# Kernel tuning notes

Hardware: AMD Instinct MI355X
Metric: run time of the kernel (lower is better)

Reference implementation:

```python
import jax, jax.numpy as jnp
import numpy as np

# Dims
B_, L_, IN_ = 16, 8192, 57
DM, DS, HD, EXP, NL, OUT = 64, 32, 32, 2, 2, 6
DI = EXP * DM            # 128 inner dim
NH = DI // HD            # 4 heads
DPROJ = 2 * DI + 2 * DS + NH  # z, x, B, C, dt


def setup_inputs() -> dict:
    key = jax.random.key(0)
    ks = jax.random.split(key, 8)
    def rn(k, shape, scale=0.02):
        return jax.random.normal(k, shape, dtype=jnp.float32) * scale
    return {
        "x": jax.random.normal(ks[0], (B_, L_, IN_), dtype=jnp.float32),
        "W_in": rn(ks[1], (IN_, DM)),
        "b_in": jnp.zeros((DM,), jnp.float32),
        "in_proj_W": rn(ks[2], (NL, DM, DPROJ)),
        "in_proj_b": jnp.zeros((NL, DPROJ), jnp.float32),
        "A_log": jnp.log(jnp.broadcast_to(jnp.arange(1, NH + 1, dtype=jnp.float32), (NL, NH))),
        "D": jnp.ones((NL, NH), jnp.float32),
        "dt_bias": rn(ks[3], (NL, NH), 0.1),
        "out_proj_W": rn(ks[4], (NL, DI, DM)),
        "out_proj_b": jnp.zeros((NL, DM), jnp.float32),
        "cls_W": rn(ks[5], (DM, OUT)),
        "cls_b": jnp.zeros((OUT,), jnp.float32),
    }


def _mamba_layer(x, W, b, A_log, D, dt_bias, Wo, bo):
    """SISO Mamba3-style selective scan block. x: [B, L, DM]."""
    Bsz, L, _ = x.shape
    zxbcdt = x @ W + b                               # [B, L, DPROJ]
    z, xin, Bm, Cm, dt = jnp.split(
        zxbcdt, [DI, 2 * DI, 2 * DI + DS, 2 * DI + 2 * DS], axis=-1)
    dt = jax.nn.softplus(dt + dt_bias)               # [B, L, NH]
    A = -jnp.exp(A_log)                              # [NH], per-head scalar (SISO)
    xin = jax.nn.silu(xin).reshape(Bsz, L, NH, HD)   # [B, L, NH, HD]
    Bm = jax.nn.silu(Bm)                             # [B, L, DS]
    Cm = jax.nn.silu(Cm)                             # [B, L, DS]
    decay = jnp.exp(dt * A)                          # [B, L, NH]

    def step(h, inp):
        # h: [B, NH, HD, DS]
        xt, bt, ct, dtt, dect = inp
        h = dect[:, :, None, None] * h + (dtt[:, :, None] * xt)[..., None] * bt[:, None, None, :]
        yt = jnp.einsum('bhpn,bn->bhp', h, ct)       # [B, NH, HD]
        return h, yt

    h0 = jnp.zeros((Bsz, NH, HD, DS), x.dtype)
    xs = (jnp.moveaxis(xin, 1, 0), jnp.moveaxis(Bm, 1, 0), jnp.moveaxis(Cm, 1, 0),
          jnp.moveaxis(dt, 1, 0), jnp.moveaxis(decay, 1, 0))
    _, ys = jax.lax.scan(step, h0, xs)               # [L, B, NH, HD]
    y = jnp.moveaxis(ys, 0, 1) + D[None, None, :, None] * xin
    y = y.reshape(Bsz, L, DI) * jax.nn.silu(z)       # gated output
    return y @ Wo + bo                               # [B, L, DM]


def reference(x, W_in, b_in, in_proj_W, in_proj_b, A_log, D, dt_bias,
              out_proj_W, out_proj_b, cls_W, cls_b):
    h = x @ W_in + b_in                              # linear_in
    for l in range(NL):                              # residual Mamba stack
        h = h + _mamba_layer(h, in_proj_W[l], in_proj_b[l], A_log[l], D[l],
                             dt_bias[l], out_proj_W[l], out_proj_b[l])
    pooled = h.mean(axis=1)                          # AdaptiveAvgPool1d(1)
    return pooled @ cls_W + cls_b                    # classifier [B, OUT]
```

## Files before the change

### kernel.cpp

```cpp
#include <hip/hip_runtime.h>

#define BSZ   16
#define LSEQ  8192
#define DMDL  64
#define DSD   32
#define HDD   32
#define NHD   4
#define DIN   128
#define NLAY  2
#define NOUTC 6
#define DPRJ  324
#define QC    64
#define NCH   128
#define NT21  21

typedef __attribute__((ext_vector_type(8))) short bf16x8;
typedef __attribute__((ext_vector_type(4))) float f32x4;

__device__ float          g_h0[BSZ*LSEQ*DMDL];
__device__ unsigned short g_xy[BSZ*LSEQ*DIN];
__device__ unsigned short g_Ba[BSZ*LSEQ*DSD];
__device__ unsigned short g_Ca[BSZ*LSEQ*DSD];
__device__ float          g_dt[BSZ*LSEQ*NHD];
__device__ float          g_pc[BSZ*LSEQ*NHD];
__device__ float          g_cS[BSZ*NCH*NHD*HDD*DSD];
__device__ unsigned short g_Hb[BSZ*NCH*NHD*HDD*DSD];
__device__ float          g_cL[BSZ*NCH*NHD];
__device__ float          g_ppc[BSZ*NCH*DMDL];
__device__ unsigned short g_wf[NLAY*NT21*2*64*8];
__device__ unsigned short g_wo[NLAY*4*4*64*8];

__device__ __forceinline__ float silu_f(float v){ return v / (1.0f + __expf(-v)); }
__device__ __forceinline__ float softplus_f(float v){ return (v > 15.0f) ? v : __logf(1.0f + __expf(v)); }
__device__ __forceinline__ unsigned short f2bf(float f){
  union { float f; unsigned u; } v; v.f = f;
  unsigned r = v.u + 0x7FFFu + ((v.u >> 16) & 1u);
  return (unsigned short)(r >> 16);
}
__device__ __forceinline__ float bf2f(unsigned short h){
  union { unsigned u; float f; } v; v.u = ((unsigned)h) << 16;
  return v.f;
}

__global__ __launch_bounds__(256) void k_linin(
    const float* __restrict__ x, const float* __restrict__ W,
    const float* __restrict__ bias)
{
  __shared__ float xs[64*60];
  __shared__ float wl[57*64];
  const int tid = threadIdx.x;
  const long tb = (long)blockIdx.x * 64;
  for (int i = tid; i < 64*57; i += 256){
    int t = i / 57, k = i - t*57;
    xs[t*60 + k] = x[tb*57 + i];
  }
  for (int i = tid; i < 57*64; i += 256) wl[i] = W[i];
  __syncthreads();
  const int t0 = (tid >> 4) * 4, d0 = (tid & 15) * 4;
  float acc[4][4];
  #pragma unroll
  for (int i = 0; i < 4; ++i)
    #pragma unroll
    for (int j = 0; j < 4; ++j) acc[i][j] = 0.f;
  for (int k = 0; k < 57; ++k){
    float4 w4 = *(const float4*)&wl[k*64 + d0];
    float wv[4] = {w4.x, w4.y, w4.z, w4.w};
    #pragma unroll
    for (int i = 0; i < 4; ++i){
      float xv = xs[(t0+i)*60 + k];
      #pragma unroll
      for (int j = 0; j < 4; ++j) acc[i][j] += xv * wv[j];
    }
  }
  float4 b4 = *(const float4*)&bias[d0];
  float bv[4] = {b4.x, b4.y, b4.z, b4.w};
  #pragma unroll
  for (int i = 0; i < 4; ++i){
    float4 o;
    o.x = acc[i][0] + bv[0]; o.y = acc[i][1] + bv[1];
    o.z = acc[i][2] + bv[2]; o.w = acc[i][3] + bv[3];
    *(float4*)&g_h0[(tb + t0 + i)*64 + d0] = o;
  }
}

__global__ __launch_bounds__(128) void k_wprep(const float* __restrict__ W)
{
  const int nt = blockIdx.x;
  const int l  = blockIdx.y;
  const int ks = threadIdx.x >> 6, lane = threadIdx.x & 63;
  const float* Wl = W + (long)l*64*DPRJ;
  const int n  = nt*16 + (lane & 15);
  const int k0 = ks*32 + (lane >> 4)*8;
  unsigned short v[8];
  #pragma unroll
  for (int j = 0; j < 8; ++j)
    v[j] = (n < DPRJ) ? f2bf(Wl[(k0 + j)*DPRJ + n]) : (unsigned short)0;
  unsigned short* d = &g_wf[((((long)l*NT21 + nt)*2 + ks)*64 + lane)*8];
  *(ushort4*)&d[0] = make_ushort4(v[0], v[1], v[2], v[3]);
  *(ushort4*)&d[4] = make_ushort4(v[4], v[5], v[6], v[7]);
}

__global__ __launch_bounds__(64) void k_wprep2(const float* __restrict__ Wo)
{
  const int nt = blockIdx.x >> 2, ks = blockIdx.x & 3, l = blockIdx.y;
  const int lane = threadIdx.x;
  const int n  = nt*16 + (lane & 15);
  const int k0 = ks*32 + (lane >> 4)*8;
  const float* Wl = Wo + (long)l*128*64;
  unsigned short* d = &g_wo[((((long)l*4 + nt)*4 + ks)*64 + lane)*8];
  unsigned short v[8];
  #pragma unroll
  for (int j = 0; j < 8; ++j) v[j] = f2bf(Wl[(k0 + j)*64 + n]);
  *(ushort4*)&d[0] = make_ushort4(v[0], v[1], v[2], v[3]);
  *(ushort4*)&d[4] = make_ushort4(v[4], v[5], v[6], v[7]);
}

#define OP 136
__global__ __launch_bounds__(256) void k_proj(
    const float* __restrict__ bias, const float* __restrict__ dt_bias, int l)
{
  __shared__ __align__(16) unsigned short Afr[8*2*64*8];
  __shared__ __align__(16) unsigned short Obuf[128*OP];
  const int tid = threadIdx.x;
  const long tb = (long)blockIdx.x * 128;
  #pragma unroll
  for (int r = 0; r < 4; ++r){
    const int c = tid + 256*r;
    const int t = c >> 3, k8 = c & 7;
    float4 f0 = *(const float4*)&g_h0[(tb + t)*64 + k8*8];
    float4 f1 = *(const float4*)&g_h0[(tb + t)*64 + k8*8 + 4];
    const int mt = t >> 4, ks = k8 >> 2, q = k8 & 3, ln = (t & 15) + 16*q;
    unsigned short* d = &Afr[(((mt*2 + ks)*64) + ln)*8];
    *(ushort4*)&d[0] = make_ushort4(f2bf(f0.x), f2bf(f0.y), f2bf(f0.z), f2bf(f0.w));
    *(ushort4*)&d[4] = make_ushort4(f2bf(f1.x), f2bf(f1.y), f2bf(f1.z), f2bf(f1.w));
  }
  __syncthreads();
  const int w = tid >> 6, lane = tid & 63;
  const int colq = lane & 15, rowq = lane >> 4;
  bf16x8 a[2][2];
  #pragma unroll
  for (int m = 0; m < 2; ++m)
    #pragma unroll
    for (int ks = 0; ks < 2; ++ks)
      a[m][ks] = *(const bf16x8*)&Afr[((((2*w + m)*2 + ks)*64) + lane)*8];
  const float* bl = bias + (long)l*DPRJ;
  const unsigned short* wf = &g_wf[(long)l*NT21*2*64*8];
  #pragma unroll
  for (int nti = 0; nti < 8; ++nti){
    const int nt = 8 + nti;
    bf16x8 b0 = *(const bf16x8*)&wf[((nt*2 + 0)*64 + lane)*8];
    bf16x8 b1 = *(const bf16x8*)&wf[((nt*2 + 1)*64 + lane)*8];
    const float b = bl[nt*16 + colq];
    #pragma unroll
    for (int m = 0; m < 2; ++m){
      f32x4 acc = {0.f, 0.f, 0.f, 0.f};
      acc = __builtin_amdgcn_mfma_f32_16x16x32_bf16(a[m][0], b0, acc, 0, 0, 0);
      acc = __builtin_amdgcn_mfma_f32_16x16x32_bf16(a[m][1], b1, acc, 0, 0, 0);
      const int tbase = (2*w + m)*16 + rowq*4;
      const int ocol = nti*16 + colq;
      #pragma unroll
      for (int r = 0; r < 4; ++r)
        Obuf[(tbase + r)*OP + ocol] = f2bf(silu_f(acc[r] + b));
    }
  }
  __syncthreads();
  #pragma unroll
  for (int it = 0; it < 8; ++it){
    const int i = tid + 256*it;
    const int t = i >> 4, c0 = (i & 15) * 8;
    *(uint4*)&g_xy[(tb + t)*128 + c0] = *(const uint4*)&Obuf[t*OP + c0];
  }
  __syncthreads();
  #pragma unroll
  for (int nti = 0; nti < 4; ++nti){
    const int nt = 16 + nti;
    bf16x8 b0 = *(const bf16x8*)&wf[((nt*2 + 0)*64 + lane)*8];
    bf16x8 b1 = *(const bf16x8*)&wf[((nt*2 + 1)*64 + lane)*8];
    const float b = bl[nt*16 + colq];
    #pragma unroll
    for (int m = 0; m < 2; ++m){
      f32x4 acc = {0.f, 0.f, 0.f, 0.f};
      acc = __builtin_amdgcn_mfma_f32_16x16x32_bf16(a[m][0], b0, acc, 0, 0, 0);
      acc = __builtin_amdgcn_mfma_f32_16x16x32_bf16(a[m][1], b1, acc, 0, 0, 0);
      const int tbase = (2*w + m)*16 + rowq*4;
      const int ocol = nti*16 + colq;
      #pragma unroll
      for (int r = 0; r < 4; ++r)
        Obuf[(tbase + r)*OP + ocol] = f2bf(silu_f(acc[r] + b));
    }
  }
  {
    bf16x8 b0 = *(const bf16x8*)&wf[((20*2 + 0)*64 + lane)*8];
    bf16x8 b1 = *(const bf16x8*)&wf[((20*2 + 1)*64 + lane)*8];
    #pragma unroll
    for (int m = 0; m < 2; ++m){
      f32x4 acc = {0.f, 0.f, 0.f, 0.f};
      acc = __builtin_amdgcn_mfma_f32_16x16x32_bf16(a[m][0], b0, acc, 0, 0, 0);
      acc = __builtin_amdgcn_mfma_f32_16x16x32_bf16(a[m][1], b1, acc, 0, 0, 0);
      if (colq < 4){
        const int tbase = (2*w + m)*16 + rowq*4;
        const float b = bl[320 + colq] + dt_bias[l*4 + colq];
        #pragma unroll
        for (int r = 0; r < 4; ++r)
          g_dt[(tb + tbase + r)*4 + colq] = softplus_f(acc[r] + b);
      }
    }
  }
  __syncthreads();
  #pragma unroll
  for (int it = 0; it < 4; ++it){
    const int i = tid + 256*it;
    const int t = i >> 3, k = i & 7;
    const int c0 = (k & 3) * 8;
    if (k < 4){
      *(uint4*)&g_Ba[(tb + t)*32 + c0] = *(const uint4*)&Obuf[t*OP + c0];
    } else {
      *(uint4*)&g_Ca[(tb + t)*32 + c0] = *(const uint4*)&Obuf[t*OP + 32 + c0];
    }
  }
}

#define SB 40
#define ST 72
__global__ __launch_bounds__(256) void k_s1(
    const float* __restrict__ A_log, const float* __restrict__ Dp, int l)
{
  __shared__ __align__(16) unsigned short u_bc[2*64*SB];
  __shared__ __align__(16) unsigned short Bbt[32*ST];
  __shared__ __align__(16) unsigned short Mb[64*ST];
  __shared__ float Sl[4*64];
  __shared__ float dts[4*64];
  __shared__ float wls[4*64];
  const int tid = threadIdx.x;
  const int cI = blockIdx.x, b = blockIdx.y;
  const long tb = (long)b*LSEQ + (long)cI*QC;
  unsigned short* Bb = u_bc;
  unsigned short* Cb = u_bc + 64*SB;
  for (int i = tid; i < 512; i += 256){
    const int s = i >> 3, n0 = (i & 7) * 4;
    ushort4 bu = *(const ushort4*)&g_Ba[(tb + s)*32 + n0];
    ushort4 cu = *(const ushort4*)&g_Ca[(tb + s)*32 + n0];
    *(ushort4*)&Bb[s*SB + n0] = bu;
    *(ushort4*)&Cb[s*SB + n0] = cu;
    Bbt[(n0    )*ST + s] = bu.x;
    Bbt[(n0 + 1)*ST + s] = bu.y;
    Bbt[(n0 + 2)*ST + s] = bu.z;
    Bbt[(n0 + 3)*ST + s] = bu.w;
  }
  {
    const int h = tid >> 6, t = tid & 63;
    const float Ah = -__expf(A_log[l*4 + h]);
    const float v = g_dt[(tb + t)*4 + h];
    float x = v * Ah;
    #pragma unroll
    for (int d = 1; d < 64; d <<= 1){
      float y = __shfl_up(x, d);
      if (t >= d) x += y;
    }
    Sl[h*64 + t] = x;
    dts[h*64 + t] = v;
    const float send = __shfl(x, 63);
    wls[h*64 + t] = __expf(send - x) * v;
    if (t == 63) g_cL[((long)b*NCH + cI)*4 + h] = x;
    g_pc[(tb + t)*4 + h] = __expf(x);
  }
  __syncthreads();
  const int w = tid >> 6, lane = tid & 63;
  const int colq = lane & 15, rowq = lane >> 4;
  float Greg[3][4];
  int Gmt[3], Gst[3];
  #pragma unroll
  for (int rep = 0; rep < 3; ++rep){
    const int k = w + rep*4;
    if (k < 10){
      const int mt = (k >= 6) ? 3 : ((k >= 3) ? 2 : ((k >= 1) ? 1 : 0));
      const int st = k - mt*(mt+1)/2;
      Gmt[rep] = mt; Gst[rep] = st;
      bf16x8 af = *(const bf16x8*)&Cb[(mt*16 + colq)*SB + rowq*8];
      bf16x8 bf = *(const bf16x8*)&Bb[(st*16 + colq)*SB + rowq*8];
      f32x4 acc = {0.f, 0.f, 0.f, 0.f};
      acc = __builtin_amdgcn_mfma_f32_16x16x32_bf16(af, bf, acc, 0, 0, 0);
      #pragma unroll
      for (int r = 0; r < 4; ++r) Greg[rep][r] = acc[r];
    } else { Gmt[rep] = -1; Gst[rep] = 0; }
  }
  #pragma unroll
  for (int rep = 0; rep < 2; ++rep){
    const int k = w + rep*4;
    if (k < 6){
      const int mt = (k < 3) ? 0 : ((k < 5) ? 1 : 2);
      const int st = (k < 3) ? (k + 1) : ((k < 5) ? (k - 1) : 3);
      #pragma unroll
      for (int r = 0; r < 4; ++r)
        Mb[(mt*16 + rowq*4 + r)*ST + st*16 + colq] = 0;
    }
  }
  unsigned short* Xt  = u_bc;
  unsigned short* Xwt = u_bc + 32*ST;
  for (int h = 0; h < NHD; ++h){
    __syncthreads();
    for (int i = tid; i < 512; i += 256){
      const int s = i >> 3, p0 = (i & 7) * 4;
      ushort4 u = *(const ushort4*)&g_xy[(tb + s)*128 + h*32 + p0];
      const float wv = wls[h*64 + s];
      Xt[(p0    )*ST + s] = u.x;  Xwt[(p0    )*ST + s] = f2bf(wv * bf2f(u.x));
      Xt[(p0 + 1)*ST + s] = u.y;  Xwt[(p0 + 1)*ST + s] = f2bf(wv * bf2f(u.y));
      Xt[(p0 + 2)*ST + s] = u.z;  Xwt[(p0 + 2)*ST + s] = f2bf(wv * bf2f(u.z));
      Xt[(p0 + 3)*ST + s] = u.w;  Xwt[(p0 + 3)*ST + s] = f2bf(wv * bf2f(u.w));
    }
    #pragma unroll
    for (int rep = 0; rep < 3; ++rep){
      if (Gmt[rep] >= 0){
        const int mt = Gmt[rep], st = Gst[rep];
        const int s = st*16 + colq;
        const float sls = Sl[h*64 + s];
        const float dv = dts[h*64 + s];
        #pragma unroll
        for (int r = 0; r < 4; ++r){
          const int t = mt*16 + rowq*4 + r;
          const float m = (s <= t) ? __expf(Sl[h*64 + t] - sls) * dv * Greg[rep][r] : 0.f;
          Mb[t*ST + s] = f2bf(m);
        }
      }
    }
    __syncthreads();
    const float Dh = Dp[l*4 + h];
    {
      bf16x8 a0 = *(const bf16x8*)&Mb[(w*16 + colq)*ST + rowq*8];
      bf16x8 a1 = *(const bf16x8*)&Mb[(w*16 + colq)*ST + 32 + rowq*8];
      #pragma unroll
      for (int nt = 0; nt < 2; ++nt){
        bf16x8 b0 = *(const bf16x8*)&Xt[(nt*16 + colq)*ST + rowq*8];
        bf16x8 b1 = *(const bf16x8*)&Xt[(nt*16 + colq)*ST + 32 + rowq*8];
        f32x4 acc = {0.f, 0.f, 0.f, 0.f};
        acc = __builtin_amdgcn_mfma_f32_16x16x32_bf16(a0, b0, acc, 0, 0, 0);
        acc = __builtin_amdgcn_mfma_f32_16x16x32_bf16(a1, b1, acc, 0, 0, 0);
        const int p = nt*16 + colq;
        #pragma unroll
        for (int r = 0; r < 4; ++r){
          const int t = w*16 + rowq*4 + r;
          const float xv = bf2f(Xt[p*ST + t]);
          g_xy[(tb + t)*128 + h*32 + p] = f2bf(acc[r] + Dh*xv);
        }
      }
    }
    {
      const int mt = w & 1, nt = w >> 1;
      bf16x8 a0 = *(const bf16x8*)&Xwt[(mt*16 + colq)*ST + rowq*8];
      bf16x8 a1 = *(const bf16x8*)&Xwt[(mt*16 + colq)*ST + 32 + rowq*8];
      bf16x8 b0 = *(const bf16x8*)&Bbt[(nt*16 + colq)*ST + rowq*8];
      bf16x8 b1 = *(const bf16x8*)&Bbt[(nt*16 + colq)*ST + 32 + rowq*8];
      f32x4 acc = {0.f, 0.f, 0.f, 0.f};
      acc = __builtin_amdgcn_mfma_f32_16x16x32_bf16(a0, b0, acc, 0, 0, 0);
      acc = __builtin_amdgcn_mfma_f32_16x16x32_bf16(a1, b1, acc, 0, 0, 0);
      const long base = (((long)b*NCH + cI)*NHD + h)*(HDD*DSD);
      const int n = nt*16 + colq;
      #pragma unroll
      for (int r = 0; r < 4; ++r){
        const int p = mt*16 + rowq*4 + r;
        g_cS[base + p*32 + n] = acc[r];
      }
    }
  }
}

__global__ __launch_bounds__(128) void k_s2()
{
  const int h = blockIdx.x >> 3, seg = blockIdx.x & 7, b = blockIdx.y;
  const int idx = seg*128 + threadIdx.x;
  float H = 0.f;
  for (int c = 0; c < NCH; ++c){
    const long o = (((long)b*NCH + c)*NHD + h)*1024 + idx;
    const float cs = g_cS[o];
    const float lg = g_cL[((long)b*NCH + c)*4 + h];
    g_Hb[o] = f2bf(H);
    H = __expf(lg) * H + cs;
  }
}

__global__ __launch_bounds__(256) void k_s3(
    const float* __restrict__ ipb, const float* __restrict__ bo, int l, int finalLayer)
{
  __shared__ __align__(16) unsigned short Hb[128*40];
  __shared__ __align__(16) unsigned short Cb[64*40];
  __shared__ __align__(16) unsigned short gl[64*136];
  __shared__ float pcl[4*64];
  __shared__ float csum[4*64];
  const int tid = threadIdx.x;
  const int cI = blockIdx.x, b = blockIdx.y;
  const long tb = (long)b*LSEQ + (long)cI*QC;
  const long hbase = (((long)b*NCH + cI)*NHD)*(long)(HDD*DSD);
  for (int i = tid; i < 512; i += 256){
    const int hp = i >> 2, n0 = (i & 3) * 8;
    *(uint4*)&Hb[hp*40 + n0] = *(const uint4*)&g_Hb[hbase + hp*32 + n0];
  }
  for (int i = tid; i < 512; i += 256){
    const int t = i >> 3, n0 = (i & 7) * 4;
    *(ushort4*)&Cb[t*40 + n0] = *(const ushort4*)&g_Ca[(tb + t)*32 + n0];
  }
  { int t = tid >> 2, h = tid & 3; pcl[h*64 + t] = g_pc[(tb + t)*4 + h]; }
  __syncthreads();
  const int w = tid >> 6, lane = tid & 63;
  const int colq = lane & 15, rowq = lane >> 4;
  const float* blz = ipb + (long)l*DPRJ;
  const unsigned short* wfz = &g_wf[(long)l*NT21*2*64*8];
  {
    const long tok0 = tb + w*16 + colq;
    bf16x8 h0a, h0b;
    {
      float4 f0 = *(const float4*)&g_h0[tok0*64 + rowq*8];
      float4 f1 = *(const float4*)&g_h0[tok0*64 + rowq*8 + 4];
      float4 f2 = *(const float4*)&g_h0[tok0*64 + 32 + rowq*8];
      float4 f3 = *(const float4*)&g_h0[tok0*64 + 32 + rowq*8 + 4];
      union { bf16x8 v; unsigned short u[8]; } ca, cb2;
      ca.u[0]=f2bf(f0.x); ca.u[1]=f2bf(f0.y); ca.u[2]=f2bf(f0.z); ca.u[3]=f2bf(f0.w);
      ca.u[4]=f2bf(f1.x); ca.u[5]=f2bf(f1.y); ca.u[6]=f2bf(f1.z); ca.u[7]=f2bf(f1.w);
      cb2.u[0]=f2bf(f2.x); cb2.u[1]=f2bf(f2.y); cb2.u[2]=f2bf(f2.z); cb2.u[3]=f2bf(f2.w);
      cb2.u[4]=f2bf(f3.x); cb2.u[5]=f2bf(f3.y); cb2.u[6]=f2bf(f3.z); cb2.u[7]=f2bf(f3.w);
      h0a = ca.v; h0b = cb2.v;
    }
    bf16x8 a = *(const bf16x8*)&Cb[(w*16 + colq)*40 + rowq*8];
    #pragma unroll
    for (int nt = 0; nt < 8; ++nt){
      bf16x8 bfr = *(const bf16x8*)&Hb[(nt*16 + colq)*40 + rowq*8];
      f32x4 acc = {0.f, 0.f, 0.f, 0.f};
      acc = __builtin_amdgcn_mfma_f32_16x16x32_bf16(a, bfr, acc, 0, 0, 0);
      bf16x8 bz0 = *(const bf16x8*)&wfz[((nt*2 + 0)*64 + lane)*8];
      bf16x8 bz1 = *(const bf16x8*)&wfz[((nt*2 + 1)*64 + lane)*8];
      f32x4 zac = {0.f, 0.f, 0.f, 0.f};
      zac = __builtin_amdgcn_mfma_f32_16x16x32_bf16(h0a, bz0, zac, 0, 0, 0);
      zac = __builtin_amdgcn_mfma_f32_16x16x32_bf16(h0b, bz1, zac, 0, 0, 0);
      const int hp = nt*16 + colq;
      const int h = hp >> 5;
      const float zb = blz[hp];
      #pragma unroll
      for (int r = 0; r < 4; ++r){
        const int t = w*16 + rowq*4 + r;
        const long tok = tb + t;
        const float v = pcl[h*64 + t] * acc[r] + bf2f(g_xy[tok*128 + hp]);
        gl[t*136 + hp] = f2bf(v * silu_f(zac[r] + zb));
      }
    }
  }
  __syncthreads();
  const unsigned short* wo = &g_wo[(long)l*4*4*512];
  #pragma unroll
  for (int nt2 = 0; nt2 < 4; ++nt2){
    f32x4 acc = {0.f, 0.f, 0.f, 0.f};
    #pragma unroll
    for (int ks = 0; ks < 4; ++ks){
      bf16x8 a = *(const bf16x8*)&gl[(w*16 + colq)*136 + ks*32 + rowq*8];
      bf16x8 bfr = *(const bf16x8*)&wo[(nt2*4 + ks)*512 + lane*8];
      acc = __builtin_amdgcn_mfma_f32_16x16x32_bf16(a, bfr, acc, 0, 0, 0);
    }
    const int dm = nt2*16 + colq;
    const float bb = bo[l*64 + dm];
    float part = 0.f;
    #pragma unroll
    for (int r = 0; r < 4; ++r){
      const int t = w*16 + rowq*4 + r;
      const long tok = tb + t;
      const float o = acc[r] + bb + g_h0[tok*64 + dm];
      g_h0[tok*64 + dm] = o;
      part += o;
    }
    if (finalLayer){
      part += __shfl_xor(part, 16);
      part += __shfl_xor(part, 32);
      if (rowq == 0) csum[w*64 + dm] = part;
    }
  }
  if (finalLayer){
    __syncthreads();
    if (tid < 64){
      g_ppc[((long)b*NCH + cI)*64 + tid] =
        csum[tid] + csum[64 + tid] + csum[128 + tid] + csum[192 + tid];
    }
  }
}

__global__ __launch_bounds__(64) void k_pool2(
    const float* __restrict__ cW, const float* __restrict__ cb,
    float* __restrict__ out)
{
  __shared__ float pl[64];
  const int b = blockIdx.x, tid = threadIdx.x;
  float s = 0.f;
  for (int c = 0; c < NCH; ++c) s += g_ppc[((long)b*NCH + c)*64 + tid];
  pl[tid] = s * (1.0f / 8192.0f);
  __syncthreads();
  if (tid < NOUTC){
    float acc = cb[tid];
    for (int dm = 0; dm < 64; ++dm) acc += pl[dm] * cW[dm*NOUTC + tid];
    out[b*NOUTC + tid] = acc;
  }
}

extern "C" void kernel_launch(void* const* d_in, const int* in_sizes, int n_in,
                              void* d_out, int out_size, void* d_ws, size_t ws_size,
                              hipStream_t stream)
{
  const float* x      = (const float*)d_in[0];
  const float* W_in   = (const float*)d_in[1];
  const float* b_in   = (const float*)d_in[2];
  const float* ipW    = (const float*)d_in[3];
  const float* ipb    = (const float*)d_in[4];
  const float* A_log  = (const float*)d_in[5];
  const float* Dp     = (const float*)d_in[6];
  const float* dtb    = (const float*)d_in[7];
  const float* opW    = (const float*)d_in[8];
  const float* opb    = (const float*)d_in[9];
  const float* clsW   = (const float*)d_in[10];
  const float* clsb   = (const float*)d_in[11];
  float* out = (float*)d_out;
  (void)d_ws; (void)ws_size;

  k_wprep<<<dim3(NT21, NLAY), 128, 0, stream>>>(ipW);
  k_wprep2<<<dim3(16, NLAY), 64, 0, stream>>>(opW);
  k_linin<<<2048, 256, 0, stream>>>(x, W_in, b_in);
  for (int l = 0; l < NLAY; ++l){
    k_proj<<<1024, 256, 0, stream>>>(ipb, dtb, l);
    k_s1<<<dim3(NCH, BSZ), 256, 0, stream>>>(A_log, Dp, l);
    k_s2<<<dim3(32, BSZ), 128, 0, stream>>>();
    k_s3<<<dim3(NCH, BSZ), 256, 0, stream>>>(ipb, opb, l, (l == NLAY-1) ? 1 : 0);
  }
  k_pool2<<<BSZ, 64, 0, stream>>>(clsW, clsb, out);
}
```

Baseline: 355.0 us.

## Swizzle k_s1 LDS layouts, double-buffer per-head tiles, widen k_linin tile

k_linin now covers 128 timesteps per block. It loads x with float4 reads into a transposed LDS tile and gives each thread a 4x8 output tile, which lowers launch count and scalar LDS traffic. In k_s1 the Xt, Bbt and Mb tiles use an XOR-style swizzled layout to cut LDS bank conflicts. Mb and Xt are double-buffered across heads, so one barrier per head is removed and the next head's x is prefetched from global into registers. The separate Xwt tile is dropped: the weighted X fragment is built in registers from the Xt fragment already loaded for the y MFMA. The cost is more LDS use and register pressure in k_s1.

Result: faster. 340.6 us (-4.1%).

```diff
diff --git a/kernel.cpp b/kernel.cpp
--- a/kernel.cpp
+++ b/kernel.cpp
@@ -42,44 +42,61 @@
   return v.f;
 }
 
+#define LSTR 132
 __global__ __launch_bounds__(256) void k_linin(
     const float* __restrict__ x, const float* __restrict__ W,
     const float* __restrict__ bias)
 {
-  __shared__ float xs[64*60];
+  __shared__ float xt[57*LSTR];
   __shared__ float wl[57*64];
   const int tid = threadIdx.x;
-  const long tb = (long)blockIdx.x * 64;
-  for (int i = tid; i < 64*57; i += 256){
-    int t = i / 57, k = i - t*57;
-    xs[t*60 + k] = x[tb*57 + i];
-  }
-  for (int i = tid; i < 57*64; i += 256) wl[i] = W[i];
-  __syncthreads();
-  const int t0 = (tid >> 4) * 4, d0 = (tid & 15) * 4;
-  float acc[4][4];
+  const long tb = (long)blockIdx.x * 128;
+  for (int i = tid; i < 912; i += 256)
+    *(float4*)&wl[i*4] = *(const float4*)&W[i*4];
+  for (int i = tid; i < 1824; i += 256){
+    float4 v = *(const float4*)&x[tb*57 + (long)i*4];
+    const int e = i*4;
+    int t0 = e / 57;
+    int k0 = e - t0*57;
+    float vv[4] = {v.x, v.y, v.z, v.w};
+    #pragma unroll
+    for (int j = 0; j < 4; ++j){
+      int t = t0, k = k0 + j;
+      if (k >= 57){ t += 1; k -= 57; }
+      xt[k*LSTR + t] = vv[j];
+    }
+  }
+  __syncthreads();
+  const int d0 = (tid & 7) * 8;
+  const int t0 = (tid >> 3) * 4;
+  float acc[4][8];
   #pragma unroll
   for (int i = 0; i < 4; ++i)
     #pragma unroll
-    for (int j = 0; j < 4; ++j) acc[i][j] = 0.f;
+    for (int j = 0; j < 8; ++j) acc[i][j] = 0.f;
+  #pragma unroll 4
   for (int k = 0; k < 57; ++k){
-    float4 w4 = *(const float4*)&wl[k*64 + d0];
-    float wv[4] = {w4.x, w4.y, w4.z, w4.w};
-    #pragma unroll
-    for (int i = 0; i < 4; ++i){
-      float xv = xs[(t0+i)*60 + k];
-      #pragma unroll
-      for (int j = 0; j < 4; ++j) acc[i][j] += xv * wv[j];
-    }
-  }
-  float4 b4 = *(const float4*)&bias[d0];
-  float bv[4] = {b4.x, b4.y, b4.z, b4.w};
+    float4 xv4 = *(const float4*)&xt[k*LSTR + t0];
+    float4 w0  = *(const float4*)&wl[k*64 + d0];
+    float4 w1  = *(const float4*)&wl[k*64 + d0 + 4];
+    float xv[4] = {xv4.x, xv4.y, xv4.z, xv4.w};
+    float wv[8] = {w0.x, w0.y, w0.z, w0.w, w1.x, w1.y, w1.z, w1.w};
+    #pragma unroll
+    for (int i = 0; i < 4; ++i)
+      #pragma unroll
+      for (int j = 0; j < 8; ++j) acc[i][j] += xv[i] * wv[j];
+  }
+  float4 bb0 = *(const float4*)&bias[d0];
+  float4 bb1 = *(const float4*)&bias[d0 + 4];
   #pragma unroll
   for (int i = 0; i < 4; ++i){
-    float4 o;
-    o.x = acc[i][0] + bv[0]; o.y = acc[i][1] + bv[1];
-    o.z = acc[i][2] + bv[2]; o.w = acc[i][3] + bv[3];
-    *(float4*)&g_h0[(tb + t0 + i)*64 + d0] = o;
+    float4 o0, o1;
+    o0.x = acc[i][0] + bb0.x; o0.y = acc[i][1] + bb0.y;
+    o0.z = acc[i][2] + bb0.z; o0.w = acc[i][3] + bb0.w;
+    o1.x = acc[i][4] + bb1.x; o1.y = acc[i][5] + bb1.y;
+    o1.z = acc[i][6] + bb1.z; o1.w = acc[i][7] + bb1.w;
+    *(float4*)&g_h0[(tb + t0 + i)*64 + d0]     = o0;
+    *(float4*)&g_h0[(tb + t0 + i)*64 + d0 + 4] = o1;
   }
 }
 
@@ -222,12 +239,18 @@
 
 #define SB 40
 #define ST 72
+__device__ __forceinline__ int xsw(int p, int s){
+  return p*ST + (((((s) >> 3) + ((p) >> 2)) & 7) << 3) + ((s) & 7);
+}
+__device__ __forceinline__ int xsw8(int p, int blk){
+  return p*ST + (((((blk)) + ((p) >> 2)) & 7) << 3);
+}
 __global__ __launch_bounds__(256) void k_s1(
     const float* __restrict__ A_log, const float* __restrict__ Dp, int l)
 {
   __shared__ __align__(16) unsigned short u_bc[2*64*SB];
   __shared__ __align__(16) unsigned short Bbt[32*ST];
-  __shared__ __align__(16) unsigned short Mb[64*ST];
+  __shared__ __align__(16) unsigned short Mb[2*64*ST];
   __shared__ float Sl[4*64];
   __shared__ float dts[4*64];
   __shared__ float wls[4*64];
@@ -236,16 +259,17 @@
   const long tb = (long)b*LSEQ + (long)cI*QC;
   unsigned short* Bb = u_bc;
   unsigned short* Cb = u_bc + 64*SB;
+  const int s0 = tid >> 3, p40 = (tid & 7) * 4;
   for (int i = tid; i < 512; i += 256){
     const int s = i >> 3, n0 = (i & 7) * 4;
     ushort4 bu = *(const ushort4*)&g_Ba[(tb + s)*32 + n0];
     ushort4 cu = *(const ushort4*)&g_Ca[(tb + s)*32 + n0];
     *(ushort4*)&Bb[s*SB + n0] = bu;
     *(ushort4*)&Cb[s*SB + n0] = cu;
-    Bbt[(n0    )*ST + s] = bu.x;
-    Bbt[(n0 + 1)*ST + s] = bu.y;
-    Bbt[(n0 + 2)*ST + s] = bu.z;
-    Bbt[(n0 + 3)*ST + s] = bu.w;
+    Bbt[xsw(n0    , s)] = bu.x;
+    Bbt[xsw(n0 + 1, s)] = bu.y;
+    Bbt[xsw(n0 + 2, s)] = bu.z;
+    Bbt[xsw(n0 + 3, s)] = bu.w;
   }
   {
     const int h = tid >> 6, t = tid & 63;
@@ -264,6 +288,8 @@
     if (t == 63) g_cL[((long)b*NCH + cI)*4 + h] = x;
     g_pc[(tb + t)*4 + h] = __expf(x);
   }
+  ushort4 xr0 = *(const ushort4*)&g_xy[(tb + s0)*128 + p40];
+  ushort4 xr1 = *(const ushort4*)&g_xy[(tb + s0 + 32)*128 + p40];
   __syncthreads();
   const int w = tid >> 6, lane = tid & 63;
   const int colq = lane & 15, rowq = lane >> 4;
@@ -291,23 +317,27 @@
       const int mt = (k < 3) ? 0 : ((k < 5) ? 1 : 2);
       const int st = (k < 3) ? (k + 1) : ((k < 5) ? (k - 1) : 3);
       #pragma unroll
-      for (int r = 0; r < 4; ++r)
-        Mb[(mt*16 + rowq*4 + r)*ST + st*16 + colq] = 0;
-    }
-  }
-  unsigned short* Xt  = u_bc;
-  unsigned short* Xwt = u_bc + 32*ST;
+      for (int r = 0; r < 4; ++r){
+        const int t = mt*16 + rowq*4 + r, s = st*16 + colq;
+        Mb[xsw(t, s)] = 0;
+        Mb[64*ST + xsw(t, s)] = 0;
+      }
+    }
+  }
+  __syncthreads();
+  unsigned short* Xt0 = u_bc;
+  unsigned short* Xt1 = u_bc + 32*ST;
   for (int h = 0; h < NHD; ++h){
-    __syncthreads();
-    for (int i = tid; i < 512; i += 256){
-      const int s = i >> 3, p0 = (i & 7) * 4;
-      ushort4 u = *(const ushort4*)&g_xy[(tb + s)*128 + h*32 + p0];
-      const float wv = wls[h*64 + s];
-      Xt[(p0    )*ST + s] = u.x;  Xwt[(p0    )*ST + s] = f2bf(wv * bf2f(u.x));
-      Xt[(p0 + 1)*ST + s] = u.y;  Xwt[(p0 + 1)*ST + s] = f2bf(wv * bf2f(u.y));
-      Xt[(p0 + 2)*ST + s] = u.z;  Xwt[(p0 + 2)*ST + s] = f2bf(wv * bf2f(u.z));
-      Xt[(p0 + 3)*ST + s] = u.w;  Xwt[(p0 + 3)*ST + s] = f2bf(wv * bf2f(u.w));
-    }
+    unsigned short* Xt  = (h & 1) ? Xt1 : Xt0;
+    unsigned short* Mbh = Mb + (h & 1)*64*ST;
+    Xt[xsw(p40    , s0)] = xr0.x;
+    Xt[xsw(p40 + 1, s0)] = xr0.y;
+    Xt[xsw(p40 + 2, s0)] = xr0.z;
+    Xt[xsw(p40 + 3, s0)] = xr0.w;
+    Xt[xsw(p40    , s0 + 32)] = xr1.x;
+    Xt[xsw(p40 + 1, s0 + 32)] = xr1.y;
+    Xt[xsw(p40 + 2, s0 + 32)] = xr1.z;
+    Xt[xsw(p40 + 3, s0 + 32)] = xr1.w;
     #pragma unroll
     for (int rep = 0; rep < 3; ++rep){
       if (Gmt[rep] >= 0){
@@ -319,42 +349,51 @@
         for (int r = 0; r < 4; ++r){
           const int t = mt*16 + rowq*4 + r;
           const float m = (s <= t) ? __expf(Sl[h*64 + t] - sls) * dv * Greg[rep][r] : 0.f;
-          Mb[t*ST + s] = f2bf(m);
+          Mbh[xsw(t, s)] = f2bf(m);
         }
       }
     }
     __syncthreads();
+    if (h < 3){
+      xr0 = *(const ushort4*)&g_xy[(tb + s0)*128 + (h + 1)*32 + p40];
+      xr1 = *(const ushort4*)&g_xy[(tb + s0 + 32)*128 + (h + 1)*32 + p40];
+    }
     const float Dh = Dp[l*4 + h];
-    {
-      bf16x8 a0 = *(const bf16x8*)&Mb[(w*16 + colq)*ST + rowq*8];
-      bf16x8 a1 = *(const bf16x8*)&Mb[(w*16 + colq)*ST + 32 + rowq*8];
-      #pragma unroll
-      for (int nt = 0; nt < 2; ++nt){
-        bf16x8 b0 = *(const bf16x8*)&Xt[(nt*16 + colq)*ST + rowq*8];
-        bf16x8 b1 = *(const bf16x8*)&Xt[(nt*16 + colq)*ST + 32 + rowq*8];
-        f32x4 acc = {0.f, 0.f, 0.f, 0.f};
-        acc = __builtin_amdgcn_mfma_f32_16x16x32_bf16(a0, b0, acc, 0, 0, 0);
-        acc = __builtin_amdgcn_mfma_f32_16x16x32_bf16(a1, b1, acc, 0, 0, 0);
-        const int p = nt*16 + colq;
-        #pragma unroll
-        for (int r = 0; r < 4; ++r){
-          const int t = w*16 + rowq*4 + r;
-          const float xv = bf2f(Xt[p*ST + t]);
-          g_xy[(tb + t)*128 + h*32 + p] = f2bf(acc[r] + Dh*xv);
-        }
-      }
-    }
-    {
-      const int mt = w & 1, nt = w >> 1;
-      bf16x8 a0 = *(const bf16x8*)&Xwt[(mt*16 + colq)*ST + rowq*8];
-      bf16x8 a1 = *(const bf16x8*)&Xwt[(mt*16 + colq)*ST + 32 + rowq*8];
-      bf16x8 b0 = *(const bf16x8*)&Bbt[(nt*16 + colq)*ST + rowq*8];
-      bf16x8 b1 = *(const bf16x8*)&Bbt[(nt*16 + colq)*ST + 32 + rowq*8];
+    bf16x8 a0 = *(const bf16x8*)&Mbh[xsw8(w*16 + colq, rowq)];
+    bf16x8 a1 = *(const bf16x8*)&Mbh[xsw8(w*16 + colq, rowq + 4)];
+    bf16x8 xb0, xb1;
+    #pragma unroll
+    for (int nt = 0; nt < 2; ++nt){
+      bf16x8 b0 = *(const bf16x8*)&Xt[xsw8(nt*16 + colq, rowq)];
+      bf16x8 b1 = *(const bf16x8*)&Xt[xsw8(nt*16 + colq, rowq + 4)];
+      if (nt == (w & 1)){ xb0 = b0; xb1 = b1; }
       f32x4 acc = {0.f, 0.f, 0.f, 0.f};
       acc = __builtin_amdgcn_mfma_f32_16x16x32_bf16(a0, b0, acc, 0, 0, 0);
       acc = __builtin_amdgcn_mfma_f32_16x16x32_bf16(a1, b1, acc, 0, 0, 0);
+      const int p = nt*16 + colq;
+      #pragma unroll
+      for (int r = 0; r < 4; ++r){
+        const int t = w*16 + rowq*4 + r;
+        const float xv = bf2f(Xt[xsw(p, t)]);
+        g_xy[(tb + t)*128 + h*32 + p] = f2bf(acc[r] + Dh*xv);
+      }
+    }
+    {
+      union { bf16x8 v; unsigned short u[8]; } sx0, sx1, sa0, sa1;
+      sx0.v = xb0; sx1.v = xb1;
+      #pragma unroll
+      for (int j = 0; j < 8; ++j){
+        sa0.u[j] = f2bf(bf2f(sx0.u[j]) * wls[h*64 + rowq*8 + j]);
+        sa1.u[j] = f2bf(bf2f(sx1.u[j]) * wls[h*64 + 32 + rowq*8 + j]);
+      }
+      const int mt = w & 1, nt2 = w >> 1;
+      bf16x8 bb0 = *(const bf16x8*)&Bbt[xsw8(nt2*16 + colq, rowq)];
+      bf16x8 bb1 = *(const bf16x8*)&Bbt[xsw8(nt2*16 + colq, rowq + 4)];
+      f32x4 acc = {0.f, 0.f, 0.f, 0.f};
+      acc = __builtin_amdgcn_mfma_f32_16x16x32_bf16(sa0.v, bb0, acc, 0, 0, 0);
+      acc = __builtin_amdgcn_mfma_f32_16x16x32_bf16(sa1.v, bb1, acc, 0, 0, 0);
       const long base = (((long)b*NCH + cI)*NHD + h)*(HDD*DSD);
-      const int n = nt*16 + colq;
+      const int n = nt2*16 + colq;
       #pragma unroll
       for (int r = 0; r < 4; ++r){
         const int p = mt*16 + rowq*4 + r;
@@ -517,7 +556,7 @@
 
   k_wprep<<<dim3(NT21, NLAY), 128, 0, stream>>>(ipW);
   k_wprep2<<<dim3(16, NLAY), 64, 0, stream>>>(opW);
-  k_linin<<<2048, 256, 0, stream>>>(x, W_in, b_in);
+  k_linin<<<1024, 256, 0, stream>>>(x, W_in, b_in);
   for (int l = 0; l < NLAY; ++l){
     k_proj<<<1024, 256, 0, stream>>>(ipb, dtb, l);
     k_s1<<<dim3(NCH, BSZ), 256, 0, stream>>>(A_log, Dp, l);
```
